# Performance work log

Hardware: AMD Instinct MI355X
Metric: run time of the kernel (lower is better)

## Reference

```python
import jax, jax.numpy as jnp
import numpy as np

D_MODEL = 768
D_INNER = 1536
D_STATE = 16
D_CONV = 4
DT_RANK = 48
N_LAYER = 4
VOCAB = 32000
B, L = 2, 1024


def rmsnorm(x, w, eps=1e-5):
    return x * jax.lax.rsqrt(jnp.mean(x * x, axis=-1, keepdims=True) + eps) * w


def depthwise_causal_conv(u, w):
    # u: (b, l, d_in), w: (d_in, k). torch pads both sides then truncates to l,
    # which equals left-pad by k-1 (causal).
    b, l, d = u.shape
    k = w.shape[1]
    up = jnp.pad(u, ((0, 0), (k - 1, 0), (0, 0)))
    out = jnp.zeros_like(u)
    for i in range(k):
        out = out + up[:, i:i + l, :] * w[:, i]
    return out


def selective_scan(u, delta, A, Bm, C, Dp):
    # u,delta: (b,l,d_in); A: (d_in,n); Bm,C: (b,l,n); Dp: (d_in,)
    dA = jnp.exp(delta[..., None] * A)                      # (b,l,d,n)
    dBu = delta[..., None] * Bm[:, :, None, :] * u[..., None]

    def step(h, inp):
        dA_t, dBu_t, C_t = inp
        h = dA_t * h + dBu_t                                 # (b,d,n)
        y = jnp.einsum('bdn,bn->bd', h, C_t)
        return h, y

    h0 = jnp.zeros_like(dA[:, 0])
    xs = (jnp.moveaxis(dA, 1, 0), jnp.moveaxis(dBu, 1, 0), jnp.moveaxis(C, 1, 0))
    _, ys = jax.lax.scan(step, h0, xs)                       # (l,b,d)
    return jnp.moveaxis(ys, 0, 1) + u * Dp


def setup_inputs() -> dict:
    key = jax.random.key(0)
    ks = jax.random.split(key, 16)
    s = lambda fan: 1.0 / np.sqrt(fan)
    inp = {}
    inp['text_input'] = jax.random.randint(ks[0], (B, L), 0, VOCAB)
    inp['visual_input'] = jax.random.normal(ks[1], (B, L, D_MODEL), dtype=jnp.float32)
    inp['embedding'] = jax.random.normal(ks[2], (VOCAB, D_MODEL), dtype=jnp.float32) * 0.02
    inp['norm_w'] = jnp.ones((N_LAYER, D_MODEL), dtype=jnp.float32)
    inp['norm_f_w'] = jnp.ones((D_MODEL,), dtype=jnp.float32)
    inp['in_proj_w'] = jax.random.normal(ks[3], (N_LAYER, 2 * D_INNER, D_MODEL)) * s(D_MODEL)
    inp['in_proj2_w'] = jax.random.normal(ks[4], (N_LAYER, D_INNER, D_MODEL)) * s(D_MODEL)
    inp['conv_w'] = jax.random.normal(ks[5], (N_LAYER, D_INNER, D_CONV)) * s(D_CONV)
    inp['conv_b'] = jax.random.normal(ks[6], (N_LAYER, D_INNER)) * 0.01
    inp['x_proj_w'] = jax.random.normal(ks[7], (N_LAYER, DT_RANK + D_STATE, D_INNER)) * s(D_INNER)
    inp['c_proj_w'] = jax.random.normal(ks[8], (N_LAYER, D_STATE, D_INNER)) * s(D_INNER)
    inp['dt_proj_w'] = jax.random.normal(ks[9], (N_LAYER, D_INNER, DT_RANK)) * s(DT_RANK)
    inp['dt_proj_b'] = jax.random.normal(ks[10], (N_LAYER, D_INNER)) * 0.01
    A = jnp.tile(jnp.arange(1, D_STATE + 1, dtype=jnp.float32)[None, :], (D_INNER, 1))
    inp['A_log'] = jnp.tile(jnp.log(A)[None], (N_LAYER, 1, 1))
    inp['D'] = jnp.ones((N_LAYER, D_INNER), dtype=jnp.float32)
    inp['out_proj_w'] = jax.random.normal(ks[11], (N_LAYER, D_MODEL, D_INNER)) * s(D_INNER)
    return inp


def reference(text_input, visual_input, embedding, norm_w, norm_f_w, in_proj_w,
              in_proj2_w, conv_w, conv_b, x_proj_w, c_proj_w, dt_proj_w,
              dt_proj_b, A_log, D, out_proj_w):
    x = embedding[text_input]  # (b,l,d_model)
    n_layer = A_log.shape[0]
    l = x.shape[1]
    for i in range(n_layer):
        q = rmsnorm(x, norm_w[i])
        v = rmsnorm(visual_input, norm_w[i])
        xr = q @ in_proj_w[i].T                               # (b,l,2*d_inner)
        vin = v @ in_proj2_w[i].T                             # (b,l,d_inner)
        t, res = jnp.split(xr, 2, axis=-1)
        t = depthwise_causal_conv(t, conv_w[i]) + conv_b[i]
        t = jax.nn.silu(t)
        # ssm
        A = -jnp.exp(A_log[i])
        x_dbl = t @ x_proj_w[i].T                             # (b,l,dt_rank+n)
        delta, Bm = jnp.split(x_dbl, [DT_RANK], axis=-1)
        C = vin @ c_proj_w[i].T                               # (b,l,n)
        delta = jax.nn.softplus(delta @ dt_proj_w[i].T + dt_proj_b[i])
        y = selective_scan(t, delta, A, Bm, C, D[i])
        y = y * jax.nn.silu(res)
        x = y @ out_proj_w[i].T + x
    x = rmsnorm(x, norm_f_w)
    return x @ embedding.T  # tied lm_head -> (b,l,vocab)
```

## Files before the change

kernel.cpp:

```cpp
#include <hip/hip_runtime.h>
#include <hip/hip_bf16.h>
#include <math.h>

#define B_ 2
#define L_ 1024
#define DM 768
#define DI 1536
#define DS 16
#define DR 48
#define NL 4
#define VOC 32000
#define BL (B_*L_)
#define NCH 32
#define LCH (L_/NCH)
#define KSPLIT 4
#define NXD 80

typedef __attribute__((ext_vector_type(8))) short short8;
typedef __attribute__((ext_vector_type(4))) float f32x4;

__device__ __forceinline__ float sigmoidf_(float x){ return 1.f/(1.f+expf(-x)); }
__device__ __forceinline__ float siluf_(float x){ return x*sigmoidf_(x); }
__device__ __forceinline__ float softplusf_(float x){ return fmaxf(x,0.f) + log1pf(expf(-fabsf(x))); }
__device__ __forceinline__ unsigned short f2bf(float f){
    unsigned u = __float_as_uint(f);
    u += 0x7FFFu + ((u >> 16) & 1u);
    return (unsigned short)(u >> 16);
}
__device__ __forceinline__ float bf2f(unsigned short h){
    return __uint_as_float((unsigned)h << 16);
}
__device__ __forceinline__ void gload_lds16(const unsigned short* g, unsigned short* l){
    __builtin_amdgcn_global_load_lds(
        (const __attribute__((address_space(1))) void*)g,
        (__attribute__((address_space(3))) void*)l, 16, 0, 0);
}

__global__ void cast_bf16_kernel(const float* __restrict__ in, unsigned short* __restrict__ out, int n4)
{
    for (int i = blockIdx.x*256 + threadIdx.x; i < n4; i += gridDim.x*256) {
        float4 v = ((const float4*)in)[i];
        ushort4 o;
        o.x = f2bf(v.x); o.y = f2bf(v.y); o.z = f2bf(v.z); o.w = f2bf(v.w);
        ((ushort4*)out)[i] = o;
    }
}

__global__ void cast_pair3_kernel(
    const float* __restrict__ s1, unsigned short* __restrict__ h1, unsigned short* __restrict__ l1, int n1,
    const float* __restrict__ s2, unsigned short* __restrict__ h2, unsigned short* __restrict__ l2, int n2,
    const float* __restrict__ s3, unsigned short* __restrict__ h3, unsigned short* __restrict__ l3, int n3)
{
    int total = n1 + n2 + n3;
    for (int i = blockIdx.x*256 + threadIdx.x; i < total; i += gridDim.x*256) {
        const float* s; unsigned short *h, *l; int j;
        if (i < n1)           { s = s1; h = h1; l = l1; j = i; }
        else if (i < n1 + n2) { s = s2; h = h2; l = l2; j = i - n1; }
        else                  { s = s3; h = h3; l = l3; j = i - n1 - n2; }
        float4 v = ((const float4*)s)[j];
        ushort4 hh, ll;
        hh.x = f2bf(v.x); ll.x = f2bf(v.x - bf2f(hh.x));
        hh.y = f2bf(v.y); ll.y = f2bf(v.y - bf2f(hh.y));
        hh.z = f2bf(v.z); ll.z = f2bf(v.z - bf2f(hh.z));
        hh.w = f2bf(v.w); ll.w = f2bf(v.w - bf2f(hh.w));
        ((ushort4*)h)[j] = hh;
        ((ushort4*)l)[j] = ll;
    }
}

__global__ void embed_kernel(const int* __restrict__ idx, const float* __restrict__ emb,
                             float* __restrict__ x)
{
    int i = blockIdx.x*256 + threadIdx.x;
    if (i >= BL*DM) return;
    int c = i % DM; int bl = i / DM;
    x[i] = emb[(size_t)idx[bl]*DM + c];
}

__global__ void rmsnorm_bf_kernel(const float* __restrict__ in, const float* __restrict__ w,
                                  unsigned short* __restrict__ out)
{
    int row = blockIdx.x;
    const float* xr = in + (size_t)row*DM;
    float ss = 0.f;
    for (int c = threadIdx.x; c < DM; c += 256) { float v = xr[c]; ss += v*v; }
    #pragma unroll
    for (int o = 32; o > 0; o >>= 1) ss += __shfl_down(ss, o, 64);
    __shared__ float red[4];
    if ((threadIdx.x & 63) == 0) red[threadIdx.x >> 6] = ss;
    __syncthreads();
    float tot = red[0] + red[1] + red[2] + red[3];
    float scale = rsqrtf(tot * (1.f/DM) + 1e-5f);
    for (int c = threadIdx.x; c < DM; c += 256)
        out[(size_t)row*DM + c] = f2bf(xr[c]*scale*w[c]);
}

__global__ void rmsnorm_dual_kernel(const float* __restrict__ x, const float* __restrict__ vis,
                                    const float* __restrict__ w,
                                    unsigned short* __restrict__ qh, unsigned short* __restrict__ ql,
                                    unsigned short* __restrict__ vh, unsigned short* __restrict__ vl)
{
    int row = blockIdx.x;
    bool first = row < BL;
    int r = first ? row : row - BL;
    const float* xr = (first ? x : vis) + (size_t)r*DM;
    unsigned short* oh = (first ? qh : vh) + (size_t)r*DM;
    unsigned short* ol = (first ? ql : vl) + (size_t)r*DM;
    float ss = 0.f;
    for (int c = threadIdx.x; c < DM; c += 256) { float v = xr[c]; ss += v*v; }
    #pragma unroll
    for (int o = 32; o > 0; o >>= 1) ss += __shfl_down(ss, o, 64);
    __shared__ float red[4];
    if ((threadIdx.x & 63) == 0) red[threadIdx.x >> 6] = ss;
    __syncthreads();
    float tot = red[0] + red[1] + red[2] + red[3];
    float scale = rsqrtf(tot * (1.f/DM) + 1e-5f);
    for (int c = threadIdx.x; c < DM; c += 256) {
        float v = xr[c]*scale*w[c];
        unsigned short h = f2bf(v);
        oh[c] = h;
        ol[c] = f2bf(v - bf2f(h));
    }
}

__global__ __launch_bounds__(256) void gemm_head(
    const unsigned short* __restrict__ A, int lda,
    const unsigned short* __restrict__ W, int ldb,
    float* __restrict__ C, int ldc, int K)
{
    __shared__ unsigned short As[128*64];
    __shared__ unsigned short Bs[128*64];
    const int tid = threadIdx.x;

    int nwg  = gridDim.x*gridDim.y;
    int flat = blockIdx.y*gridDim.x + blockIdx.x;
    if ((nwg & 7) == 0) {
        int q = nwg >> 3;
        flat = (flat & 7)*q + (flat >> 3);
    }
    const int bm = (flat % gridDim.x)*128;
    const int bn = (flat / gridDim.x)*128;

    const int l  = tid & 63;
    const int w  = tid >> 6;
    const int wr = (w >> 1)*64, wc = (w & 1)*64;
    const int lr = l & 15, lg = l >> 4;

    f32x4 zero4 = {0.f, 0.f, 0.f, 0.f};
    f32x4 acc[4][4];
    #pragma unroll
    for (int m = 0; m < 4; m++)
        #pragma unroll
        for (int n = 0; n < 4; n++) acc[m][n] = zero4;

    for (int k0 = 0; k0 < K; k0 += 64) {
        __syncthreads();
        #pragma unroll
        for (int i = 0; i < 4; i++) {
            int c   = i*256 + tid;
            int row = c >> 3;
            int kb  = c & 7;
            int kbs = (kb ^ (row & 7)) << 3;
            gload_lds16(A + (size_t)(bm+row)*lda + k0 + kbs, &As[c*8]);
            gload_lds16(W + (size_t)(bn+row)*ldb + k0 + kbs, &Bs[c*8]);
        }
        __syncthreads();
        #pragma unroll
        for (int kk = 0; kk < 2; kk++) {
            short8 af[4], bfr[4];
            #pragma unroll
            for (int m = 0; m < 4; m++) {
                int row = wr + m*16 + lr;
                af[m] = *(const short8*)&As[row*64 + (((kk*4+lg) ^ (row & 7)) << 3)];
            }
            #pragma unroll
            for (int n = 0; n < 4; n++) {
                int row = wc + n*16 + lr;
                bfr[n] = *(const short8*)&Bs[row*64 + (((kk*4+lg) ^ (row & 7)) << 3)];
            }
            #pragma unroll
            for (int m = 0; m < 4; m++)
                #pragma unroll
                for (int n = 0; n < 4; n++)
                    acc[m][n] = __builtin_amdgcn_mfma_f32_16x16x32_bf16(af[m], bfr[n], acc[m][n], 0, 0, 0);
        }
    }

    #pragma unroll
    for (int m = 0; m < 4; m++)
        #pragma unroll
        for (int n = 0; n < 4; n++) {
            int col = bn + wc + n*16 + lr;
            #pragma unroll
            for (int r = 0; r < 4; r++) {
                int rowi = bm + wr + m*16 + lg*4 + r;
                __builtin_nontemporal_store(acc[m][n][r], &C[(size_t)rowi*ldc + col]);
            }
        }
}

template<int EPI>
__device__ __forceinline__ void mfma2_body(
    const unsigned short* __restrict__ Ah, const unsigned short* __restrict__ Alo, int lda,
    const unsigned short* __restrict__ Wh, const unsigned short* __restrict__ Wlo, int ldb,
    float* __restrict__ C, int ldc, const float* __restrict__ extra,
    int K, int bm, int bn,
    unsigned short* Ash, unsigned short* Asl, unsigned short* Bsh, unsigned short* Bsl)
{
    const int tid = threadIdx.x;
    const int l  = tid & 63;
    const int w  = tid >> 6;
    const int wr = (w >> 1)*64, wc = (w & 1)*64;
    const int lr = l & 15, lg = l >> 4;

    f32x4 zero4 = {0.f, 0.f, 0.f, 0.f};
    f32x4 acc[4][4];
    #pragma unroll
    for (int m = 0; m < 4; m++)
        #pragma unroll
        for (int n = 0; n < 4; n++) acc[m][n] = zero4;

    for (int k0 = 0; k0 < K; k0 += 64) {
        __syncthreads();
        #pragma unroll
        for (int i = 0; i < 4; i++) {
            int c   = i*256 + tid;
            int row = c >> 3;
            int kb  = c & 7;
            int kbs = (kb ^ (row & 7)) << 3;
            const size_t ao = (size_t)(bm+row)*lda + k0 + kbs;
            const size_t bo = (size_t)(bn+row)*ldb + k0 + kbs;
            gload_lds16(Ah  + ao, &Ash[c*8]);
            gload_lds16(Alo + ao, &Asl[c*8]);
            gload_lds16(Wh  + bo, &Bsh[c*8]);
            gload_lds16(Wlo + bo, &Bsl[c*8]);
        }
        __syncthreads();
        #pragma unroll
        for (int kk = 0; kk < 2; kk++) {
            short8 ah[4], al[4], bh[4], bl[4];
            #pragma unroll
            for (int m = 0; m < 4; m++) {
                int row = wr + m*16 + lr;
                int so  = row*64 + (((kk*4 + lg) ^ (row & 7)) << 3);
                ah[m] = *(const short8*)&Ash[so];
                al[m] = *(const short8*)&Asl[so];
            }
            #pragma unroll
            for (int n = 0; n < 4; n++) {
                int row = wc + n*16 + lr;
                int so  = row*64 + (((kk*4 + lg) ^ (row & 7)) << 3);
                bh[n] = *(const short8*)&Bsh[so];
                bl[n] = *(const short8*)&Bsl[so];
            }
            #pragma unroll
            for (int m = 0; m < 4; m++)
                #pragma unroll
                for (int n = 0; n < 4; n++) {
                    acc[m][n] = __builtin_amdgcn_mfma_f32_16x16x32_bf16(al[m], bh[n], acc[m][n], 0, 0, 0);
                    acc[m][n] = __builtin_amdgcn_mfma_f32_16x16x32_bf16(ah[m], bl[n], acc[m][n], 0, 0, 0);
                    acc[m][n] = __builtin_amdgcn_mfma_f32_16x16x32_bf16(ah[m], bh[n], acc[m][n], 0, 0, 0);
                }
        }
    }

    #pragma unroll
    for (int m = 0; m < 4; m++)
        #pragma unroll
        for (int n = 0; n < 4; n++) {
            int col = bn + wc + n*16 + lr;
            #pragma unroll
            for (int r = 0; r < 4; r++) {
                int rowi = bm + wr + m*16 + lg*4 + r;
                float v = acc[m][n][r];
                if (EPI == 1) v += extra[(size_t)rowi*ldc + col];
                C[(size_t)rowi*ldc + col] = v;
            }
        }
}

template<int EPI>
__global__ __launch_bounds__(256) void gemm_mfma2(
    const unsigned short* __restrict__ Ah, const unsigned short* __restrict__ Alo, int lda,
    const unsigned short* __restrict__ Wh, const unsigned short* __restrict__ Wlo, int ldb,
    float* __restrict__ C, int ldc, const float* __restrict__ extra, int K)
{
    __shared__ unsigned short Ash[128*64];
    __shared__ unsigned short Asl[128*64];
    __shared__ unsigned short Bsh[128*64];
    __shared__ unsigned short Bsl[128*64];
    mfma2_body<EPI>(Ah, Alo, lda, Wh, Wlo, ldb, C, ldc, extra, K,
                    blockIdx.y*128, blockIdx.x*128, Ash, Asl, Bsh, Bsl);
}

__global__ __launch_bounds__(256) void gemm_mfma2_dual(
    const unsigned short* __restrict__ Ah1, const unsigned short* __restrict__ Al1,
    const unsigned short* __restrict__ Wh1, const unsigned short* __restrict__ Wl1,
    float* __restrict__ C1, int ldc1, int nb1,
    const unsigned short* __restrict__ Ah2, const unsigned short* __restrict__ Al2,
    const unsigned short* __restrict__ Wh2, const unsigned short* __restrict__ Wl2,
    float* __restrict__ C2, int ldc2,
    int lda, int ldb, int K)
{
    __shared__ unsigned short Ash[128*64];
    __shared__ unsigned short Asl[128*64];
    __shared__ unsigned short Bsh[128*64];
    __shared__ unsigned short Bsl[128*64];
    int bx = blockIdx.x;
    if (bx < nb1)
        mfma2_body<0>(Ah1, Al1, lda, Wh1, Wl1, ldb, C1, ldc1, nullptr, K,
                      blockIdx.y*128, bx*128, Ash, Asl, Bsh, Bsl);
    else
        mfma2_body<0>(Ah2, Al2, lda, Wh2, Wl2, ldb, C2, ldc2, nullptr, K,
                      blockIdx.y*128, (bx-nb1)*128, Ash, Asl, Bsh, Bsl);
}

template<int EPI>
__global__ __launch_bounds__(256) void gemm_tile(
    const float* __restrict__ A, int lda,
    const float* __restrict__ W, int ldb,
    float* __restrict__ C, int ldc,
    const float* __restrict__ extra,
    int K)
{
    __shared__ float As[8][128];
    __shared__ float Bs[8][128];
    const int bm = blockIdx.y * 128;
    const int bn = blockIdx.x * 128;
    const int tid = threadIdx.x;
    const int lr = tid >> 1;
    const int lh = (tid & 1) * 4;
    const int tr = tid >> 4;
    const int tc = tid & 15;

    float acc[8][8];
    #pragma unroll
    for (int i = 0; i < 8; i++)
        #pragma unroll
        for (int j = 0; j < 8; j++) acc[i][j] = 0.f;

    const float* Arow = A + (size_t)(bm + lr)*lda + lh;
    const float* Wrow = W + (size_t)(bn + lr)*ldb + lh;

    for (int k0 = 0; k0 < K; k0 += 8) {
        float4 av = *(const float4*)(Arow + k0);
        float4 wv = *(const float4*)(Wrow + k0);
        __syncthreads();
        As[lh+0][lr] = av.x; As[lh+1][lr] = av.y; As[lh+2][lr] = av.z; As[lh+3][lr] = av.w;
        Bs[lh+0][lr] = wv.x; Bs[lh+1][lr] = wv.y; Bs[lh+2][lr] = wv.z; Bs[lh+3][lr] = wv.w;
        __syncthreads();
        #pragma unroll
        for (int k = 0; k < 8; k++) {
            float a[8], b[8];
            *(float4*)(a)   = *(const float4*)&As[k][tr*8];
            *(float4*)(a+4) = *(const float4*)&As[k][tr*8+4];
            *(float4*)(b)   = *(const float4*)&Bs[k][tc*8];
            *(float4*)(b+4) = *(const float4*)&Bs[k][tc*8+4];
            #pragma unroll
            for (int i = 0; i < 8; i++)
                #pragma unroll
                for (int j = 0; j < 8; j++)
                    acc[i][j] = fmaf(a[i], b[j], acc[i][j]);
        }
    }

    #pragma unroll
    for (int i = 0; i < 8; i++) {
        int row = bm + tr*8 + i;
        float* crow = C + (size_t)row*ldc + bn + tc*8;
        float v[8];
        if (EPI == 2) {
            const float* bia = extra + bn + tc*8;
            #pragma unroll
            for (int j = 0; j < 8; j++) v[j] = softplusf_(acc[i][j] + bia[j]);
        } else {
            #pragma unroll
            for (int j = 0; j < 8; j++) v[j] = acc[i][j];
        }
        *(float4*)(crow)   = make_float4(v[0],v[1],v[2],v[3]);
        *(float4*)(crow+4) = make_float4(v[4],v[5],v[6],v[7]);
    }
}

__global__ __launch_bounds__(256) void gemm_skinny2(
    const float* __restrict__ A1, const float* __restrict__ A2, int lda,
    const float* __restrict__ W1, const float* __restrict__ W2, int ldb,
    float* __restrict__ partial, int K)
{
    int klen = K / gridDim.z;
    int kbeg = blockIdx.z * klen;
    __shared__ float As[64][36];
    __shared__ float Ws[16][36];
    int tid = threadIdx.x;
    int bx = blockIdx.x;
    bool isC = (bx == 4);
    const float* A = isC ? A2 : A1;
    const float* W = isC ? W2 : W1;
    int bn = isC ? 0 : bx*16;
    int colbase = isC ? 64 : bx*16;
    int bm = blockIdx.y*64;
    int ar = tid >> 2, ak = (tid & 3)*8;
    int wr = tid >> 4, wk = (tid & 15)*2;
    int tr = tid >> 4, tc = tid & 15;

    float acc[4] = {0.f,0.f,0.f,0.f};
    for (int k0 = kbeg; k0 < kbeg + klen; k0 += 32) {
        float4 a0 = *(const float4*)(A + (size_t)(bm+ar)*lda + k0 + ak);
        float4 a1 = *(const float4*)(A + (size_t)(bm+ar)*lda + k0 + ak + 4);
        float2 wv = *(const float2*)(W + (size_t)(bn+wr)*ldb + k0 + wk);
        __syncthreads();
        *(float4*)&As[ar][ak]   = a0;
        *(float4*)&As[ar][ak+4] = a1;
        Ws[wr][wk] = wv.x; Ws[wr][wk+1] = wv.y;
        __syncthreads();
        #pragma unroll
        for (int k = 0; k < 32; k += 4) {
            float4 wv4 = *(const float4*)&Ws[tc][k];
            #pragma unroll
            for (int i = 0; i < 4; i++) {
                float4 av4 = *(const float4*)&As[tr*4+i][k];
                acc[i] = fmaf(av4.x, wv4.x, acc[i]);
                acc[i] = fmaf(av4.y, wv4.y, acc[i]);
                acc[i] = fmaf(av4.z, wv4.z, acc[i]);
                acc[i] = fmaf(av4.w, wv4.w, acc[i]);
            }
        }
    }
    #pragma unroll
    for (int i = 0; i < 4; i++)
        partial[((size_t)blockIdx.z*BL + bm + tr*4 + i)*NXD + colbase + tc] = acc[i];
}

__global__ void reduce_splitk(const float* __restrict__ partial, float* __restrict__ out, int MN)
{
    int i = blockIdx.x*256 + threadIdx.x;
    if (i >= MN) return;
    float s = 0.f;
    #pragma unroll
    for (int z = 0; z < KSPLIT; z++) s += partial[(size_t)z*MN + i];
    out[i] = s;
}

__global__ void conv_silu_kernel(const float* __restrict__ xr, const float* __restrict__ cw,
                                 const float* __restrict__ cb, float* __restrict__ t)
{
    int i = blockIdx.x*256 + threadIdx.x;
    if (i >= BL*DI) return;
    int d = i % DI; int bl = i / DI; int l = bl % L_; int b = bl / L_;
    const float* base = xr + (size_t)b*L_*(2*DI);
    float acc = cb[d];
    #pragma unroll
    for (int q = 0; q < 4; q++) {
        int ll = l - 3 + q;
        if (ll >= 0) acc = fmaf(base[(size_t)ll*(2*DI) + d], cw[d*4+q], acc);
    }
    t[i] = siluf_(acc);
}

__global__ void scan_p1(const float* __restrict__ delta, const float* __restrict__ t,
                        const float* __restrict__ xdbl, const float* __restrict__ A_log,
                        float* __restrict__ Aprod, float* __restrict__ Bacc)
{
    int idx = blockIdx.x*256 + threadIdx.x;
    if (idx >= B_*NCH*DI) return;
    int d = idx % DI; int c = (idx/DI) % NCH; int b = idx/(DI*NCH);
    float Ad[16];
    #pragma unroll
    for (int n = 0; n < 16; n++) Ad[n] = -expf(A_log[d*16+n]);
    float P[16], S[16];
    #pragma unroll
    for (int n = 0; n < 16; n++) { P[n] = 1.f; S[n] = 0.f; }
    for (int s = 0; s < LCH; s++) {
        int bl = b*L_ + c*LCH + s;
        float dt = delta[(size_t)bl*DI + d];
        float u  = t[(size_t)bl*DI + d];
        const float4* Bp4 = (const float4*)(xdbl + (size_t)bl*NXD + 48);
        float Bv[16];
        #pragma unroll
        for (int q = 0; q < 4; q++) {
            float4 bv = Bp4[q];
            Bv[q*4+0]=bv.x; Bv[q*4+1]=bv.y; Bv[q*4+2]=bv.z; Bv[q*4+3]=bv.w;
        }
        float du = dt*u;
        #pragma unroll
        for (int n = 0; n < 16; n++) {
            float a  = expf(dt*Ad[n]);
            P[n] *= a;
            S[n] = fmaf(a, S[n], du*Bv[n]);
        }
    }
    size_t o = (size_t)idx*16;
    #pragma unroll
    for (int n = 0; n < 16; n++) { Aprod[o+n] = P[n]; Bacc[o+n] = S[n]; }
}

__global__ void scan_p2(const float* __restrict__ Aprod, const float* __restrict__ Bacc,
                        float* __restrict__ Hinit)
{
    int idx = blockIdx.x*256 + threadIdx.x;
    if (idx >= B_*DI) return;
    int d = idx % DI, b = idx / DI;
    float h[16];
    #pragma unroll
    for (int n = 0; n < 16; n++) h[n] = 0.f;
    for (int c = 0; c < NCH; c++) {
        size_t o = (((size_t)b*NCH + c)*DI + d)*16;
        #pragma unroll
        for (int n = 0; n < 16; n++) Hinit[o+n] = h[n];
        #pragma unroll
        for (int n = 0; n < 16; n++) h[n] = fmaf(Aprod[o+n], h[n], Bacc[o+n]);
    }
}

__global__ void scan_p3(const float* __restrict__ delta, const float* __restrict__ t,
                        const float* __restrict__ xdbl,
                        const float* __restrict__ A_log, const float* __restrict__ Dp,
                        const float* __restrict__ Hinit, const float* __restrict__ xr,
                        unsigned short* __restrict__ zh, unsigned short* __restrict__ zl)
{
    int idx = blockIdx.x*256 + threadIdx.x;
    if (idx >= B_*NCH*DI) return;
    int d = idx % DI; int c = (idx/DI) % NCH; int b = idx/(DI*NCH);
    float Ad[16];
    #pragma unroll
    for (int n = 0; n < 16; n++) Ad[n] = -expf(A_log[d*16+n]);
    float h[16];
    size_t ho = (size_t)idx*16;
    #pragma unroll
    for (int n = 0; n < 16; n++) h[n] = Hinit[ho+n];
    float Dd = Dp[d];
    for (int s = 0; s < LCH; s++) {
        int bl = b*L_ + c*LCH + s;
        float dt = delta[(size_t)bl*DI + d];
        float u  = t[(size_t)bl*DI + d];
        const float4* Bp4 = (const float4*)(xdbl + (size_t)bl*NXD + 48);
        const float4* Cp4 = (const float4*)(xdbl + (size_t)bl*NXD + 64);
        float Bv[16], Cv[16];
        #pragma unroll
        for (int q = 0; q < 4; q++) {
            float4 bv = Bp4[q]; float4 cv = Cp4[q];
            Bv[q*4+0]=bv.x; Bv[q*4+1]=bv.y; Bv[q*4+2]=bv.z; Bv[q*4+3]=bv.w;
            Cv[q*4+0]=cv.x; Cv[q*4+1]=cv.y; Cv[q*4+2]=cv.z; Cv[q*4+3]=cv.w;
        }
        float du = dt*u;
        float y = 0.f;
        #pragma unroll
        for (int n = 0; n < 16; n++) {
            float a = expf(dt*Ad[n]);
            h[n] = fmaf(a, h[n], du*Bv[n]);
            y = fmaf(h[n], Cv[n], y);
        }
        y = fmaf(u, Dd, y);
        float r = xr[(size_t)bl*(2*DI) + DI + d];
        float zv = y * siluf_(r);
        unsigned short hh = f2bf(zv);
        zh[(size_t)bl*DI + d] = hh;
        zl[(size_t)bl*DI + d] = f2bf(zv - bf2f(hh));
    }
}

extern "C" void kernel_launch(void* const* d_in, const int* in_sizes, int n_in,
                              void* d_out, int out_size, void* d_ws, size_t ws_size,
                              hipStream_t stream)
{
    const int*   text     = (const int*)  d_in[0];
    const float* visual   = (const float*)d_in[1];
    const float* emb      = (const float*)d_in[2];
    const float* norm_w   = (const float*)d_in[3];
    const float* norm_f_w = (const float*)d_in[4];
    const float* in_proj  = (const float*)d_in[5];
    const float* in_proj2 = (const float*)d_in[6];
    const float* conv_w   = (const float*)d_in[7];
    const float* conv_b   = (const float*)d_in[8];
    const float* x_proj   = (const float*)d_in[9];
    const float* c_proj   = (const float*)d_in[10];
    const float* dt_w     = (const float*)d_in[11];
    const float* dt_b     = (const float*)d_in[12];
    const float* A_log    = (const float*)d_in[13];
    const float* Dp       = (const float*)d_in[14];
    const float* out_proj = (const float*)d_in[15];
    float* out = (float*)d_out;

    float* ws = (float*)d_ws;
    size_t off = 0;
    float* x     = ws + off; off += (size_t)BL*DM;
    float* xr    = ws + off; off += (size_t)BL*2*DI;
    float* vin   = ws + off; off += (size_t)BL*DI;
    float* tb    = ws + off; off += (size_t)BL*DI;
    float* dl    = ws + off; off += (size_t)BL*DI;
    float* xdbl  = ws + off; off += (size_t)BL*NXD;
    float* Aprod = ws + off; off += (size_t)B_*NCH*DI*DS;
    float* Bacc  = ws + off; off += (size_t)B_*NCH*DI*DS;
    float* Hinit = ws + off; off += (size_t)B_*NCH*DI*DS;
    float* part  = ws + off; off += (size_t)KSPLIT*BL*NXD;

    unsigned short* bfb = (unsigned short*)(ws + off);
    size_t bo = 0;
    unsigned short* emb_bf = bfb + bo; bo += (size_t)VOC*DM;
    unsigned short* wA_h   = bfb + bo; bo += (size_t)2*DI*DM;
    unsigned short* wA_l   = bfb + bo; bo += (size_t)2*DI*DM;
    unsigned short* wB_h   = bfb + bo; bo += (size_t)DI*DM;
    unsigned short* wB_l   = bfb + bo; bo += (size_t)DI*DM;
    unsigned short* wO_h   = bfb + bo; bo += (size_t)DM*DI;
    unsigned short* wO_l   = bfb + bo; bo += (size_t)DM*DI;
    unsigned short* q_h    = bfb + bo; bo += (size_t)BL*DM;
    unsigned short* q_l    = bfb + bo; bo += (size_t)BL*DM;
    unsigned short* v_h    = bfb + bo; bo += (size_t)BL*DM;
    unsigned short* v_l    = bfb + bo; bo += (size_t)BL*DM;
    unsigned short* z_h    = bfb + bo; bo += (size_t)BL*DI;
    unsigned short* z_l    = bfb + bo; bo += (size_t)BL*DI;
    unsigned short* xn_bf  = bfb + bo; bo += (size_t)BL*DM;

    dim3 blk(256);
    dim3 cgrid(2048);

    cast_bf16_kernel<<<cgrid, blk, 0, stream>>>(emb, emb_bf, VOC*DM/4);

    embed_kernel<<<dim3((BL*DM)/256), blk, 0, stream>>>(text, emb, x);

    for (int i = 0; i < NL; i++) {
        const float* nw = norm_w + (size_t)i*DM;

        rmsnorm_dual_kernel<<<dim3(2*BL), blk, 0, stream>>>(
            x, visual, nw, q_h, q_l, v_h, v_l);

        cast_pair3_kernel<<<cgrid, blk, 0, stream>>>(
            in_proj  + (size_t)i*2*DI*DM, wA_h, wA_l, 2*DI*DM/4,
            in_proj2 + (size_t)i*DI*DM,   wB_h, wB_l, DI*DM/4,
            out_proj + (size_t)i*DM*DI,   wO_h, wO_l, DM*DI/4);

        gemm_mfma2_dual<<<dim3(2*DI/128 + DI/128, BL/128), blk, 0, stream>>>(
            q_h, q_l, wA_h, wA_l, xr, 2*DI, 2*DI/128,
            v_h, v_l, wB_h, wB_l, vin, DI,
            DM, DM, DM);

        conv_silu_kernel<<<dim3((BL*DI)/256), blk, 0, stream>>>(
            xr, conv_w + (size_t)i*DI*4, conv_b + (size_t)i*DI, tb);

        gemm_skinny2<<<dim3(5, BL/64, KSPLIT), blk, 0, stream>>>(
            tb, vin, DI, x_proj + (size_t)i*(DR+DS)*DI, c_proj + (size_t)i*DS*DI, DI,
            part, DI);
        reduce_splitk<<<dim3((BL*NXD)/256), blk, 0, stream>>>(part, xdbl, BL*NXD);

        gemm_tile<2><<<dim3(DI/128, BL/128), blk, 0, stream>>>(
            xdbl, NXD, dt_w + (size_t)i*DI*DR, DR, dl, DI, dt_b + (size_t)i*DI, DR);

        const float* Al = A_log + (size_t)i*DI*DS;
        scan_p1<<<dim3((B_*NCH*DI)/256), blk, 0, stream>>>(dl, tb, xdbl, Al, Aprod, Bacc);
        scan_p2<<<dim3((B_*DI+255)/256), blk, 0, stream>>>(Aprod, Bacc, Hinit);
        scan_p3<<<dim3((B_*NCH*DI)/256), blk, 0, stream>>>(dl, tb, xdbl, Al,
            Dp + (size_t)i*DI, Hinit, xr, z_h, z_l);

        gemm_mfma2<1><<<dim3(DM/128, BL/128), blk, 0, stream>>>(
            z_h, z_l, DI, wO_h, wO_l, DI, x, DM, x, DI);
    }

    rmsnorm_bf_kernel<<<dim3(BL), blk, 0, stream>>>(x, norm_f_w, xn_bf);
    gemm_head<<<dim3(BL/128, VOC/128), blk, 0, stream>>>(
        xn_bf, DM, emb_bf, DM, out, VOC, DM);
}
```

Measured before the change: 1.721 ms.

## Halve split-bf16 GEMM K tile, remap dual grid, parallelize scan pass 2

The split-bf16 MFMA GEMM body drops its K step from 64 to 32, cutting LDS per block from 64KB to 32KB so more blocks can be resident per CU, at the cost of twice as many barriers per K. The dual GEMM remaps its flat block index in groups of 8 and walks column-major so neighbouring blocks share inputs in cache. Scan pass 2 now uses one thread per (b,d,n) instead of one per (b,d), giving 16x more threads and coalesced accesses. The head GEMM swaps nontemporal stores for plain stores.

New measurement: 1.733 ms. Within noise of the previous version (+0.7%).

```diff
diff --git a/kernel.cpp b/kernel.cpp
--- a/kernel.cpp
+++ b/kernel.cpp
@@ -194,7 +194,7 @@
             #pragma unroll
             for (int r = 0; r < 4; r++) {
                 int rowi = bm + wr + m*16 + lg*4 + r;
-                __builtin_nontemporal_store(acc[m][n][r], &C[(size_t)rowi*ldc + col]);
+                C[(size_t)rowi*ldc + col] = acc[m][n][r];
             }
         }
 }
@@ -220,14 +220,14 @@
         #pragma unroll
         for (int n = 0; n < 4; n++) acc[m][n] = zero4;
 
-    for (int k0 = 0; k0 < K; k0 += 64) {
-        __syncthreads();
-        #pragma unroll
-        for (int i = 0; i < 4; i++) {
+    for (int k0 = 0; k0 < K; k0 += 32) {
+        __syncthreads();
+        #pragma unroll
+        for (int i = 0; i < 2; i++) {
             int c   = i*256 + tid;
-            int row = c >> 3;
-            int kb  = c & 7;
-            int kbs = (kb ^ (row & 7)) << 3;
+            int row = c >> 2;
+            int kb  = c & 3;
+            int kbs = (kb ^ (row & 3)) << 3;
             const size_t ao = (size_t)(bm+row)*lda + k0 + kbs;
             const size_t bo = (size_t)(bn+row)*ldb + k0 + kbs;
             gload_lds16(Ah  + ao, &Ash[c*8]);
@@ -236,32 +236,29 @@
             gload_lds16(Wlo + bo, &Bsl[c*8]);
         }
         __syncthreads();
-        #pragma unroll
-        for (int kk = 0; kk < 2; kk++) {
-            short8 ah[4], al[4], bh[4], bl[4];
-            #pragma unroll
-            for (int m = 0; m < 4; m++) {
-                int row = wr + m*16 + lr;
-                int so  = row*64 + (((kk*4 + lg) ^ (row & 7)) << 3);
-                ah[m] = *(const short8*)&Ash[so];
-                al[m] = *(const short8*)&Asl[so];
+        short8 ah[4], al[4], bh[4], bl[4];
+        #pragma unroll
+        for (int m = 0; m < 4; m++) {
+            int row = wr + m*16 + lr;
+            int so  = row*32 + ((lg ^ (row & 3)) << 3);
+            ah[m] = *(const short8*)&Ash[so];
+            al[m] = *(const short8*)&Asl[so];
+        }
+        #pragma unroll
+        for (int n = 0; n < 4; n++) {
+            int row = wc + n*16 + lr;
+            int so  = row*32 + ((lg ^ (row & 3)) << 3);
+            bh[n] = *(const short8*)&Bsh[so];
+            bl[n] = *(const short8*)&Bsl[so];
+        }
+        #pragma unroll
+        for (int m = 0; m < 4; m++)
+            #pragma unroll
+            for (int n = 0; n < 4; n++) {
+                acc[m][n] = __builtin_amdgcn_mfma_f32_16x16x32_bf16(al[m], bh[n], acc[m][n], 0, 0, 0);
+                acc[m][n] = __builtin_amdgcn_mfma_f32_16x16x32_bf16(ah[m], bl[n], acc[m][n], 0, 0, 0);
+                acc[m][n] = __builtin_amdgcn_mfma_f32_16x16x32_bf16(ah[m], bh[n], acc[m][n], 0, 0, 0);
             }
-            #pragma unroll
-            for (int n = 0; n < 4; n++) {
-                int row = wc + n*16 + lr;
-                int so  = row*64 + (((kk*4 + lg) ^ (row & 7)) << 3);
-                bh[n] = *(const short8*)&Bsh[so];
-                bl[n] = *(const short8*)&Bsl[so];
-            }
-            #pragma unroll
-            for (int m = 0; m < 4; m++)
-                #pragma unroll
-                for (int n = 0; n < 4; n++) {
-                    acc[m][n] = __builtin_amdgcn_mfma_f32_16x16x32_bf16(al[m], bh[n], acc[m][n], 0, 0, 0);
-                    acc[m][n] = __builtin_amdgcn_mfma_f32_16x16x32_bf16(ah[m], bl[n], acc[m][n], 0, 0, 0);
-                    acc[m][n] = __builtin_amdgcn_mfma_f32_16x16x32_bf16(ah[m], bh[n], acc[m][n], 0, 0, 0);
-                }
-        }
     }
 
     #pragma unroll
@@ -285,10 +282,10 @@
     const unsigned short* __restrict__ Wh, const unsigned short* __restrict__ Wlo, int ldb,
     float* __restrict__ C, int ldc, const float* __restrict__ extra, int K)
 {
-    __shared__ unsigned short Ash[128*64];
-    __shared__ unsigned short Asl[128*64];
-    __shared__ unsigned short Bsh[128*64];
-    __shared__ unsigned short Bsl[128*64];
+    __shared__ unsigned short Ash[128*32];
+    __shared__ unsigned short Asl[128*32];
+    __shared__ unsigned short Bsh[128*32];
+    __shared__ unsigned short Bsl[128*32];
     mfma2_body<EPI>(Ah, Alo, lda, Wh, Wlo, ldb, C, ldc, extra, K,
                     blockIdx.y*128, blockIdx.x*128, Ash, Asl, Bsh, Bsl);
 }
@@ -302,17 +299,24 @@
     float* __restrict__ C2, int ldc2,
     int lda, int ldb, int K)
 {
-    __shared__ unsigned short Ash[128*64];
-    __shared__ unsigned short Asl[128*64];
-    __shared__ unsigned short Bsh[128*64];
-    __shared__ unsigned short Bsl[128*64];
-    int bx = blockIdx.x;
+    __shared__ unsigned short Ash[128*32];
+    __shared__ unsigned short Asl[128*32];
+    __shared__ unsigned short Bsh[128*32];
+    __shared__ unsigned short Bsl[128*32];
+    int nwg  = gridDim.x*gridDim.y;
+    int flat = blockIdx.y*gridDim.x + blockIdx.x;
+    if ((nwg & 7) == 0) {
+        int q = nwg >> 3;
+        flat = (flat & 7)*q + (flat >> 3);
+    }
+    int by = flat % gridDim.y;
+    int bx = flat / gridDim.y;
     if (bx < nb1)
         mfma2_body<0>(Ah1, Al1, lda, Wh1, Wl1, ldb, C1, ldc1, nullptr, K,
-                      blockIdx.y*128, bx*128, Ash, Asl, Bsh, Bsl);
+                      by*128, bx*128, Ash, Asl, Bsh, Bsl);
     else
         mfma2_body<0>(Ah2, Al2, lda, Wh2, Wl2, ldb, C2, ldc2, nullptr, K,
-                      blockIdx.y*128, (bx-nb1)*128, Ash, Asl, Bsh, Bsl);
+                      by*128, (bx-nb1)*128, Ash, Asl, Bsh, Bsl);
 }
 
 template<int EPI>
@@ -498,17 +502,15 @@
                         float* __restrict__ Hinit)
 {
     int idx = blockIdx.x*256 + threadIdx.x;
-    if (idx >= B_*DI) return;
-    int d = idx % DI, b = idx / DI;
-    float h[16];
-    #pragma unroll
-    for (int n = 0; n < 16; n++) h[n] = 0.f;
+    if (idx >= B_*DI*DS) return;
+    int bd = idx >> 4;
+    int n  = idx & 15;
+    int b  = bd / DI, d = bd % DI;
+    float h = 0.f;
     for (int c = 0; c < NCH; c++) {
-        size_t o = (((size_t)b*NCH + c)*DI + d)*16;
-        #pragma unroll
-        for (int n = 0; n < 16; n++) Hinit[o+n] = h[n];
-        #pragma unroll
-        for (int n = 0; n < 16; n++) h[n] = fmaf(Aprod[o+n], h[n], Bacc[o+n]);
+        size_t o = (((size_t)b*NCH + c)*DI + d)*16 + n;
+        Hinit[o] = h;
+        h = fmaf(Aprod[o], h, Bacc[o]);
     }
 }
 
@@ -647,7 +649,7 @@
 
         const float* Al = A_log + (size_t)i*DI*DS;
         scan_p1<<<dim3((B_*NCH*DI)/256), blk, 0, stream>>>(dl, tb, xdbl, Al, Aprod, Bacc);
-        scan_p2<<<dim3((B_*DI+255)/256), blk, 0, stream>>>(Aprod, Bacc, Hinit);
+        scan_p2<<<dim3((B_*DI*DS)/256), blk, 0, stream>>>(Aprod, Bacc, Hinit);
         scan_p3<<<dim3((B_*NCH*DI)/256), blk, 0, stream>>>(dl, tb, xdbl, Al,
             Dp + (size_t)i*DI, Hinit, xr, z_h, z_l);
 
```

## Fuse chunked scan passes, merge layer prep kernels, drop split-K and head swizzle

Applied to the files above, without the earlier changes.

Merges the three chunked selective-scan kernels into one block-local kernel. Each block handles 8 channels across all 32 chunks and does the inter-chunk carry in LDS, so the Aprod/Bacc/Hinit global round trips go away. It also folds the rmsnorm and weight-cast kernels into one launch and removes split-K plus its reduce kernel from the skinny GEMM. In the LM-head GEMM it drops the XCD-aware tile swizzle and nontemporal stores and reorders the grid. The trade-off is that the scan now runs a serial 32-step carry on half the threads, and the skinny GEMM has less parallelism without split-K.

Result: faster. 1.587 ms (-7.8%).

```diff
diff --git a/kernel.cpp b/kernel.cpp
--- a/kernel.cpp
+++ b/kernel.cpp
@@ -13,8 +13,8 @@
 #define BL (B_*L_)
 #define NCH 32
 #define LCH (L_/NCH)
-#define KSPLIT 4
 #define NXD 80
+#define DTILE 8
 
 typedef __attribute__((ext_vector_type(8))) short short8;
 typedef __attribute__((ext_vector_type(4))) float f32x4;
@@ -43,28 +43,6 @@
         ushort4 o;
         o.x = f2bf(v.x); o.y = f2bf(v.y); o.z = f2bf(v.z); o.w = f2bf(v.w);
         ((ushort4*)out)[i] = o;
-    }
-}
-
-__global__ void cast_pair3_kernel(
-    const float* __restrict__ s1, unsigned short* __restrict__ h1, unsigned short* __restrict__ l1, int n1,
-    const float* __restrict__ s2, unsigned short* __restrict__ h2, unsigned short* __restrict__ l2, int n2,
-    const float* __restrict__ s3, unsigned short* __restrict__ h3, unsigned short* __restrict__ l3, int n3)
-{
-    int total = n1 + n2 + n3;
-    for (int i = blockIdx.x*256 + threadIdx.x; i < total; i += gridDim.x*256) {
-        const float* s; unsigned short *h, *l; int j;
-        if (i < n1)           { s = s1; h = h1; l = l1; j = i; }
-        else if (i < n1 + n2) { s = s2; h = h2; l = l2; j = i - n1; }
-        else                  { s = s3; h = h3; l = l3; j = i - n1 - n2; }
-        float4 v = ((const float4*)s)[j];
-        ushort4 hh, ll;
-        hh.x = f2bf(v.x); ll.x = f2bf(v.x - bf2f(hh.x));
-        hh.y = f2bf(v.y); ll.y = f2bf(v.y - bf2f(hh.y));
-        hh.z = f2bf(v.z); ll.z = f2bf(v.z - bf2f(hh.z));
-        hh.w = f2bf(v.w); ll.w = f2bf(v.w - bf2f(hh.w));
-        ((ushort4*)h)[j] = hh;
-        ((ushort4*)l)[j] = ll;
     }
 }
 
@@ -95,31 +73,53 @@
         out[(size_t)row*DM + c] = f2bf(xr[c]*scale*w[c]);
 }
 
-__global__ void rmsnorm_dual_kernel(const float* __restrict__ x, const float* __restrict__ vis,
-                                    const float* __restrict__ w,
-                                    unsigned short* __restrict__ qh, unsigned short* __restrict__ ql,
-                                    unsigned short* __restrict__ vh, unsigned short* __restrict__ vl)
-{
-    int row = blockIdx.x;
-    bool first = row < BL;
-    int r = first ? row : row - BL;
-    const float* xr = (first ? x : vis) + (size_t)r*DM;
-    unsigned short* oh = (first ? qh : vh) + (size_t)r*DM;
-    unsigned short* ol = (first ? ql : vl) + (size_t)r*DM;
-    float ss = 0.f;
-    for (int c = threadIdx.x; c < DM; c += 256) { float v = xr[c]; ss += v*v; }
-    #pragma unroll
-    for (int o = 32; o > 0; o >>= 1) ss += __shfl_down(ss, o, 64);
-    __shared__ float red[4];
-    if ((threadIdx.x & 63) == 0) red[threadIdx.x >> 6] = ss;
-    __syncthreads();
-    float tot = red[0] + red[1] + red[2] + red[3];
-    float scale = rsqrtf(tot * (1.f/DM) + 1e-5f);
-    for (int c = threadIdx.x; c < DM; c += 256) {
-        float v = xr[c]*scale*w[c];
-        unsigned short h = f2bf(v);
-        oh[c] = h;
-        ol[c] = f2bf(v - bf2f(h));
+__global__ void prep_layer(
+    const float* __restrict__ x, const float* __restrict__ vis, const float* __restrict__ w,
+    unsigned short* __restrict__ qh, unsigned short* __restrict__ ql,
+    unsigned short* __restrict__ vh, unsigned short* __restrict__ vl,
+    const float* __restrict__ s1, unsigned short* __restrict__ h1, unsigned short* __restrict__ l1, int n1,
+    const float* __restrict__ s2, unsigned short* __restrict__ h2, unsigned short* __restrict__ l2, int n2,
+    const float* __restrict__ s3, unsigned short* __restrict__ h3, unsigned short* __restrict__ l3, int n3)
+{
+    if (blockIdx.x < 2*BL) {
+        int row = blockIdx.x;
+        bool first = row < BL;
+        int r = first ? row : row - BL;
+        const float* xr = (first ? x : vis) + (size_t)r*DM;
+        unsigned short* oh = (first ? qh : vh) + (size_t)r*DM;
+        unsigned short* ol = (first ? ql : vl) + (size_t)r*DM;
+        float ss = 0.f;
+        for (int c = threadIdx.x; c < DM; c += 256) { float v = xr[c]; ss += v*v; }
+        #pragma unroll
+        for (int o = 32; o > 0; o >>= 1) ss += __shfl_down(ss, o, 64);
+        __shared__ float red[4];
+        if ((threadIdx.x & 63) == 0) red[threadIdx.x >> 6] = ss;
+        __syncthreads();
+        float tot = red[0] + red[1] + red[2] + red[3];
+        float scale = rsqrtf(tot * (1.f/DM) + 1e-5f);
+        for (int c = threadIdx.x; c < DM; c += 256) {
+            float v = xr[c]*scale*w[c];
+            unsigned short h = f2bf(v);
+            oh[c] = h;
+            ol[c] = f2bf(v - bf2f(h));
+        }
+    } else {
+        int total = n1 + n2 + n3;
+        int nblk = gridDim.x - 2*BL;
+        for (int i = (blockIdx.x - 2*BL)*256 + threadIdx.x; i < total; i += nblk*256) {
+            const float* s; unsigned short *h, *l; int j;
+            if (i < n1)           { s = s1; h = h1; l = l1; j = i; }
+            else if (i < n1 + n2) { s = s2; h = h2; l = l2; j = i - n1; }
+            else                  { s = s3; h = h3; l = l3; j = i - n1 - n2; }
+            float4 v = ((const float4*)s)[j];
+            ushort4 hh, ll;
+            hh.x = f2bf(v.x); ll.x = f2bf(v.x - bf2f(hh.x));
+            hh.y = f2bf(v.y); ll.y = f2bf(v.y - bf2f(hh.y));
+            hh.z = f2bf(v.z); ll.z = f2bf(v.z - bf2f(hh.z));
+            hh.w = f2bf(v.w); ll.w = f2bf(v.w - bf2f(hh.w));
+            ((ushort4*)h)[j] = hh;
+            ((ushort4*)l)[j] = ll;
+        }
     }
 }
 
@@ -131,16 +131,7 @@
     __shared__ unsigned short As[128*64];
     __shared__ unsigned short Bs[128*64];
     const int tid = threadIdx.x;
-
-    int nwg  = gridDim.x*gridDim.y;
-    int flat = blockIdx.y*gridDim.x + blockIdx.x;
-    if ((nwg & 7) == 0) {
-        int q = nwg >> 3;
-        flat = (flat & 7)*q + (flat >> 3);
-    }
-    const int bm = (flat % gridDim.x)*128;
-    const int bn = (flat / gridDim.x)*128;
-
+    const int bm = blockIdx.y*128, bn = blockIdx.x*128;
     const int l  = tid & 63;
     const int w  = tid >> 6;
     const int wr = (w >> 1)*64, wc = (w & 1)*64;
@@ -194,7 +185,7 @@
             #pragma unroll
             for (int r = 0; r < 4; r++) {
                 int rowi = bm + wr + m*16 + lg*4 + r;
-                __builtin_nontemporal_store(acc[m][n][r], &C[(size_t)rowi*ldc + col]);
+                C[(size_t)rowi*ldc + col] = acc[m][n][r];
             }
         }
 }
@@ -385,10 +376,8 @@
 __global__ __launch_bounds__(256) void gemm_skinny2(
     const float* __restrict__ A1, const float* __restrict__ A2, int lda,
     const float* __restrict__ W1, const float* __restrict__ W2, int ldb,
-    float* __restrict__ partial, int K)
-{
-    int klen = K / gridDim.z;
-    int kbeg = blockIdx.z * klen;
+    float* __restrict__ outx, int K)
+{
     __shared__ float As[64][36];
     __shared__ float Ws[16][36];
     int tid = threadIdx.x;
@@ -404,7 +393,7 @@
     int tr = tid >> 4, tc = tid & 15;
 
     float acc[4] = {0.f,0.f,0.f,0.f};
-    for (int k0 = kbeg; k0 < kbeg + klen; k0 += 32) {
+    for (int k0 = 0; k0 < K; k0 += 32) {
         float4 a0 = *(const float4*)(A + (size_t)(bm+ar)*lda + k0 + ak);
         float4 a1 = *(const float4*)(A + (size_t)(bm+ar)*lda + k0 + ak + 4);
         float2 wv = *(const float2*)(W + (size_t)(bn+wr)*ldb + k0 + wk);
@@ -428,17 +417,7 @@
     }
     #pragma unroll
     for (int i = 0; i < 4; i++)
-        partial[((size_t)blockIdx.z*BL + bm + tr*4 + i)*NXD + colbase + tc] = acc[i];
-}
-
-__global__ void reduce_splitk(const float* __restrict__ partial, float* __restrict__ out, int MN)
-{
-    int i = blockIdx.x*256 + threadIdx.x;
-    if (i >= MN) return;
-    float s = 0.f;
-    #pragma unroll
-    for (int z = 0; z < KSPLIT; z++) s += partial[(size_t)z*MN + i];
-    out[i] = s;
+        outx[(size_t)(bm + tr*4 + i)*NXD + colbase + tc] = acc[i];
 }
 
 __global__ void conv_silu_kernel(const float* __restrict__ xr, const float* __restrict__ cw,
@@ -457,16 +436,26 @@
     t[i] = siluf_(acc);
 }
 
-__global__ void scan_p1(const float* __restrict__ delta, const float* __restrict__ t,
-                        const float* __restrict__ xdbl, const float* __restrict__ A_log,
-                        float* __restrict__ Aprod, float* __restrict__ Bacc)
-{
-    int idx = blockIdx.x*256 + threadIdx.x;
-    if (idx >= B_*NCH*DI) return;
-    int d = idx % DI; int c = (idx/DI) % NCH; int b = idx/(DI*NCH);
+__global__ __launch_bounds__(256) void scan_fused(
+    const float* __restrict__ delta, const float* __restrict__ t,
+    const float* __restrict__ xdbl,
+    const float* __restrict__ A_log, const float* __restrict__ Dp,
+    const float* __restrict__ xr,
+    unsigned short* __restrict__ zh, unsigned short* __restrict__ zl)
+{
+    __shared__ float P_lds[256*17];
+    __shared__ float S_lds[256*17];
+    int blk = blockIdx.x;
+    int b  = blk / (DI/DTILE);
+    int d0 = (blk % (DI/DTILE))*DTILE;
+    int tid = threadIdx.x;
+    int dl = tid & 7, c = tid >> 3;
+    int d = d0 + dl;
+
     float Ad[16];
     #pragma unroll
     for (int n = 0; n < 16; n++) Ad[n] = -expf(A_log[d*16+n]);
+
     float P[16], S[16];
     #pragma unroll
     for (int n = 0; n < 16; n++) { P[n] = 1.f; S[n] = 0.f; }
@@ -484,50 +473,31 @@
         float du = dt*u;
         #pragma unroll
         for (int n = 0; n < 16; n++) {
-            float a  = expf(dt*Ad[n]);
+            float a = expf(dt*Ad[n]);
             P[n] *= a;
             S[n] = fmaf(a, S[n], du*Bv[n]);
         }
     }
-    size_t o = (size_t)idx*16;
-    #pragma unroll
-    for (int n = 0; n < 16; n++) { Aprod[o+n] = P[n]; Bacc[o+n] = S[n]; }
-}
-
-__global__ void scan_p2(const float* __restrict__ Aprod, const float* __restrict__ Bacc,
-                        float* __restrict__ Hinit)
-{
-    int idx = blockIdx.x*256 + threadIdx.x;
-    if (idx >= B_*DI) return;
-    int d = idx % DI, b = idx / DI;
+    #pragma unroll
+    for (int n = 0; n < 16; n++) { P_lds[tid*17+n] = P[n]; S_lds[tid*17+n] = S[n]; }
+    __syncthreads();
+
+    if (tid < 128) {
+        int dl2 = tid >> 4, n2 = tid & 15;
+        float h = 0.f;
+        for (int cc = 0; cc < NCH; cc++) {
+            int slot = cc*8 + dl2;
+            float p = P_lds[slot*17 + n2];
+            float s = S_lds[slot*17 + n2];
+            S_lds[slot*17 + n2] = h;
+            h = fmaf(p, h, s);
+        }
+    }
+    __syncthreads();
+
     float h[16];
     #pragma unroll
-    for (int n = 0; n < 16; n++) h[n] = 0.f;
-    for (int c = 0; c < NCH; c++) {
-        size_t o = (((size_t)b*NCH + c)*DI + d)*16;
-        #pragma unroll
-        for (int n = 0; n < 16; n++) Hinit[o+n] = h[n];
-        #pragma unroll
-        for (int n = 0; n < 16; n++) h[n] = fmaf(Aprod[o+n], h[n], Bacc[o+n]);
-    }
-}
-
-__global__ void scan_p3(const float* __restrict__ delta, const float* __restrict__ t,
-                        const float* __restrict__ xdbl,
-                        const float* __restrict__ A_log, const float* __restrict__ Dp,
-                        const float* __restrict__ Hinit, const float* __restrict__ xr,
-                        unsigned short* __restrict__ zh, unsigned short* __restrict__ zl)
-{
-    int idx = blockIdx.x*256 + threadIdx.x;
-    if (idx >= B_*NCH*DI) return;
-    int d = idx % DI; int c = (idx/DI) % NCH; int b = idx/(DI*NCH);
-    float Ad[16];
-    #pragma unroll
-    for (int n = 0; n < 16; n++) Ad[n] = -expf(A_log[d*16+n]);
-    float h[16];
-    size_t ho = (size_t)idx*16;
-    #pragma unroll
-    for (int n = 0; n < 16; n++) h[n] = Hinit[ho+n];
+    for (int n = 0; n < 16; n++) h[n] = S_lds[tid*17+n];
     float Dd = Dp[d];
     for (int s = 0; s < LCH; s++) {
         int bl = b*L_ + c*LCH + s;
@@ -589,10 +559,6 @@
     float* tb    = ws + off; off += (size_t)BL*DI;
     float* dl    = ws + off; off += (size_t)BL*DI;
     float* xdbl  = ws + off; off += (size_t)BL*NXD;
-    float* Aprod = ws + off; off += (size_t)B_*NCH*DI*DS;
-    float* Bacc  = ws + off; off += (size_t)B_*NCH*DI*DS;
-    float* Hinit = ws + off; off += (size_t)B_*NCH*DI*DS;
-    float* part  = ws + off; off += (size_t)KSPLIT*BL*NXD;
 
     unsigned short* bfb = (unsigned short*)(ws + off);
     size_t bo = 0;
@@ -612,19 +578,16 @@
     unsigned short* xn_bf  = bfb + bo; bo += (size_t)BL*DM;
 
     dim3 blk(256);
-    dim3 cgrid(2048);
-
-    cast_bf16_kernel<<<cgrid, blk, 0, stream>>>(emb, emb_bf, VOC*DM/4);
+
+    cast_bf16_kernel<<<dim3(2048), blk, 0, stream>>>(emb, emb_bf, VOC*DM/4);
 
     embed_kernel<<<dim3((BL*DM)/256), blk, 0, stream>>>(text, emb, x);
 
     for (int i = 0; i < NL; i++) {
         const float* nw = norm_w + (size_t)i*DM;
 
-        rmsnorm_dual_kernel<<<dim3(2*BL), blk, 0, stream>>>(
-            x, visual, nw, q_h, q_l, v_h, v_l);
-
-        cast_pair3_kernel<<<cgrid, blk, 0, stream>>>(
+        prep_layer<<<dim3(2*BL + 1024), blk, 0, stream>>>(
+            x, visual, nw, q_h, q_l, v_h, v_l,
             in_proj  + (size_t)i*2*DI*DM, wA_h, wA_l, 2*DI*DM/4,
             in_proj2 + (size_t)i*DI*DM,   wB_h, wB_l, DI*DM/4,
             out_proj + (size_t)i*DM*DI,   wO_h, wO_l, DM*DI/4);
@@ -637,25 +600,21 @@
         conv_silu_kernel<<<dim3((BL*DI)/256), blk, 0, stream>>>(
             xr, conv_w + (size_t)i*DI*4, conv_b + (size_t)i*DI, tb);
 
-        gemm_skinny2<<<dim3(5, BL/64, KSPLIT), blk, 0, stream>>>(
+        gemm_skinny2<<<dim3(5, BL/64), blk, 0, stream>>>(
             tb, vin, DI, x_proj + (size_t)i*(DR+DS)*DI, c_proj + (size_t)i*DS*DI, DI,
-            part, DI);
-        reduce_splitk<<<dim3((BL*NXD)/256), blk, 0, stream>>>(part, xdbl, BL*NXD);
+            xdbl, DI);
 
         gemm_tile<2><<<dim3(DI/128, BL/128), blk, 0, stream>>>(
             xdbl, NXD, dt_w + (size_t)i*DI*DR, DR, dl, DI, dt_b + (size_t)i*DI, DR);
 
-        const float* Al = A_log + (size_t)i*DI*DS;
-        scan_p1<<<dim3((B_*NCH*DI)/256), blk, 0, stream>>>(dl, tb, xdbl, Al, Aprod, Bacc);
-        scan_p2<<<dim3((B_*DI+255)/256), blk, 0, stream>>>(Aprod, Bacc, Hinit);
-        scan_p3<<<dim3((B_*NCH*DI)/256), blk, 0, stream>>>(dl, tb, xdbl, Al,
-            Dp + (size_t)i*DI, Hinit, xr, z_h, z_l);
+        scan_fused<<<dim3(B_*DI/DTILE), blk, 0, stream>>>(
+            dl, tb, xdbl, A_log + (size_t)i*DI*DS, Dp + (size_t)i*DI, xr, z_h, z_l);
 
         gemm_mfma2<1><<<dim3(DM/128, BL/128), blk, 0, stream>>>(
             z_h, z_l, DI, wO_h, wO_l, DI, x, DM, x, DI);
     }
 
     rmsnorm_bf_kernel<<<dim3(BL), blk, 0, stream>>>(x, norm_f_w, xn_bf);
-    gemm_head<<<dim3(BL/128, VOC/128), blk, 0, stream>>>(
+    gemm_head<<<dim3(VOC/128, BL/128), blk, 0, stream>>>(
         xn_bf, DM, emb_bf, DM, out, VOC, DM);
 }
```
